# Performance work log

Hardware: AMD Instinct MI355X
Metric: run time of the kernel (lower is better)

The kernel has to match this reference:

```python
import jax, jax.numpy as jnp
import numpy as np

SEP_ID = 102  # bert-base [SEP]


def setup_inputs() -> dict:
    key = jax.random.key(0)
    B, S, H, M = 64, 512, 768, 21
    k1, k2, k3, k4 = jax.random.split(key, 4)
    hidden = jax.random.normal(k1, (B, S, H), dtype=jnp.float32)  # tf1 last_hidden_state
    ids = jax.random.randint(k2, (B, S), 1000, 30000)
    sep_pos = jnp.arange(24, 24 * (M + 1), 24)  # 21 sep positions < 512
    ids = ids.at[:, sep_pos].set(SEP_ID)
    W = jax.random.normal(k3, (H, H), dtype=jnp.float32) * 0.02  # nn.Linear weight [out,in]
    b = jnp.zeros((H,), dtype=jnp.float32)
    v = jax.random.normal(k4, (H,), dtype=jnp.float32) * 0.02    # linear_value [H,1] squeezed
    return {"hidden": hidden, "input_ids": ids, "W": W, "b": b, "v": v,
            "max_sent_count": M}


def _segment_attention_pool(hidden, input_ids, W, b, v, M):
    B, S, H = hidden.shape
    sep = input_ids == SEP_ID                                 # [B,S] bool
    csum = jnp.cumsum(sep.astype(jnp.int32), axis=1)
    seg = csum - sep.astype(jnp.int32)                        # seps strictly before t
    nsep = csum[:, -1]                                        # sentences per row
    pos = jnp.arange(S)
    # sentence k = tokens strictly between sep k-1 and sep k, excluding CLS (pos 0)
    valid = (~sep) & (pos[None, :] >= 1) & (seg < nsep[:, None]) & (seg < M)

    # attention scores: tanh(x @ W.T + b) @ v
    scores = jnp.einsum('bsh,h->bs', jnp.tanh(jnp.einsum('bsh,kh->bsk', hidden, W) + b), v)

    NS = B * M + 1                                            # +1 dummy segment for invalid tokens
    fid = jnp.where(valid, jnp.arange(B)[:, None] * M + seg, B * M).reshape(-1)
    sflat = jnp.where(valid, scores, -jnp.inf).reshape(-1)

    # per-segment stable softmax
    m = jax.ops.segment_max(sflat, fid, num_segments=NS)
    m = jnp.where(jnp.isfinite(m), m, 0.0)                    # empty segments
    e = jnp.where(valid.reshape(-1), jnp.exp(sflat - m[fid]), 0.0)
    denom = jax.ops.segment_sum(e, fid, num_segments=NS)
    w = e / jnp.where(denom[fid] > 0, denom[fid], 1.0)

    sent = jax.ops.segment_sum(w[:, None] * hidden.reshape(-1, H), fid,
                               num_segments=NS)[:B * M].reshape(B, M, H)
    # rows with zero sentences fall back to the CLS embedding (original behavior)
    sent = sent.at[:, 0, :].set(jnp.where((nsep == 0)[:, None], hidden[:, 0, :], sent[:, 0, :]))
    return sent


def reference(hidden, input_ids, W, b, v, max_sent_count):
    return _segment_attention_pool(hidden, input_ids, W, b, v, max_sent_count)
```

## Files before the change

### kernel.cpp

```cpp
#include <hip/hip_runtime.h>


#define SEP_ID 102
#define Bn 64
#define Sn 512
#define Hn 768
#define Mn 21
#define BS (Bn * Sn)

typedef __attribute__((ext_vector_type(8))) short bf16x8;
typedef __attribute__((ext_vector_type(8))) unsigned short u16x8;
typedef __attribute__((ext_vector_type(4))) float f32x4;

__device__ inline unsigned short f2bf(float x) {
  unsigned int u = __builtin_bit_cast(unsigned int, x);
  u += 0x7fffu + ((u >> 16) & 1u);
  return (unsigned short)(u >> 16);
}

__device__ inline u16x8 cvt8(float4 a, float4 b) {
  u16x8 r;
  r[0] = f2bf(a.x); r[1] = f2bf(a.y); r[2] = f2bf(a.z); r[3] = f2bf(a.w);
  r[4] = f2bf(b.x); r[5] = f2bf(b.y); r[6] = f2bf(b.z); r[7] = f2bf(b.w);
  return r;
}

__device__ inline float tanh_fast(float x) {
  float e = __builtin_amdgcn_exp2f(x * 2.885390081777927f);
  return 1.f - 2.f * __builtin_amdgcn_rcpf(e + 1.f);
}

__global__ void convw_kernel(const float* __restrict__ W, unsigned short* __restrict__ WBp) {
  int c = blockIdx.x * 256 + threadIdx.x;
  int nt = c / 1536;
  int r  = c % 1536;
  int ks = r >> 6;
  int ln = r & 63;
  int col = nt * 16 + (ln & 15);
  int k0  = ks * 32 + (ln >> 4) * 8;
  const float* src = &W[col * Hn + k0];
  float4 a = *reinterpret_cast<const float4*>(src);
  float4 b = *reinterpret_cast<const float4*>(src + 4);
  *reinterpret_cast<u16x8*>(&WBp[(size_t)c * 8]) = cvt8(a, b);
}

__global__ void segscan_kernel(const int* __restrict__ ids,
                               unsigned char* __restrict__ segv,
                               int* __restrict__ nsep) {
  int b = blockIdx.x;
  int s = threadIdx.x;
  __shared__ int cs[Sn];
  int sep = (ids[b * Sn + s] == SEP_ID) ? 1 : 0;
  cs[s] = sep;
  __syncthreads();
  for (int off = 1; off < Sn; off <<= 1) {
    int add = (s >= off) ? cs[s - off] : 0;
    __syncthreads();
    cs[s] += add;
    __syncthreads();
  }
  int csum = cs[s];
  int nb = cs[Sn - 1];
  int seg = csum - sep;
  bool valid = (!sep) && (s >= 1) && (seg < nb) && (seg < Mn);
  segv[b * Sn + s] = valid ? (unsigned char)seg : (unsigned char)0xFF;
  if (s == 0) nsep[b] = nb;
}

__global__ __launch_bounds__(1024, 4) void score_gemm_kernel(
    const float* __restrict__ hid, const unsigned short* __restrict__ WBp,
    const float* __restrict__ bbias, const float* __restrict__ vvec,
    float* __restrict__ scores) {
  __shared__ __align__(16) unsigned short As[64 * 768];
  __shared__ float scpart[16][64];

  const int t = threadIdx.x;
  const size_t rowBase = (size_t)blockIdx.x * 64;
  const int wid = t >> 6, lane = t & 63;
  const int l15 = lane & 15, l4 = lane >> 4;
  const int colBase = wid * 48;

  {
    const int srow = t >> 4;
    const int scloc = t & 15;
    const float* hsrc = &hid[(rowBase + srow) * Hn + scloc * 8];
    unsigned short* const arow = &As[srow * Hn];
    const int swz = srow & 7;
    float4 p[6][2];
#pragma unroll
    for (int cc = 0; cc < 6; ++cc) {
      p[cc][0] = *reinterpret_cast<const float4*>(hsrc + cc * 128);
      p[cc][1] = *reinterpret_cast<const float4*>(hsrc + cc * 128 + 4);
    }
#pragma unroll
    for (int cc = 0; cc < 6; ++cc)
      *reinterpret_cast<u16x8*>(arow + ((cc * 16 + scloc) ^ swz) * 8) =
          cvt8(p[cc][0], p[cc][1]);
  }
  __syncthreads();

  const unsigned short* const afrow = &As[l15 * Hn];
  const int aswz = l15 & 7;
  const unsigned short* bp0 = &WBp[((size_t)(wid * 3 + 0) * 24 * 64 + lane) * 8];
  const unsigned short* bp1 = &WBp[((size_t)(wid * 3 + 1) * 24 * 64 + lane) * 8];
  const unsigned short* bp2 = &WBp[((size_t)(wid * 3 + 2) * 24 * 64 + lane) * 8];

  f32x4 acc[4][3];
#pragma unroll
  for (int mi = 0; mi < 4; ++mi)
#pragma unroll
    for (int ni = 0; ni < 3; ++ni) acc[mi][ni] = (f32x4){0.f, 0.f, 0.f, 0.f};

  bf16x8 b0[3], b1[3], b2[3];
  b0[0] = *reinterpret_cast<const bf16x8*>(bp0);
  b0[1] = *reinterpret_cast<const bf16x8*>(bp1);
  b0[2] = *reinterpret_cast<const bf16x8*>(bp2);
  b1[0] = *reinterpret_cast<const bf16x8*>(bp0 + 512);
  b1[1] = *reinterpret_cast<const bf16x8*>(bp1 + 512);
  b1[2] = *reinterpret_cast<const bf16x8*>(bp2 + 512);

#pragma unroll
  for (int kk = 0; kk < 24; ++kk) {
    bf16x8 af[4];
#pragma unroll
    for (int mi = 0; mi < 4; ++mi)
      af[mi] = *reinterpret_cast<const bf16x8*>(
          &afrow[mi * 16 * Hn + (((kk * 4 + l4)) ^ aswz) * 8]);
    if (kk + 2 < 24) {
      b2[0] = *reinterpret_cast<const bf16x8*>(bp0 + (kk + 2) * 512);
      b2[1] = *reinterpret_cast<const bf16x8*>(bp1 + (kk + 2) * 512);
      b2[2] = *reinterpret_cast<const bf16x8*>(bp2 + (kk + 2) * 512);
    }
    __builtin_amdgcn_s_setprio(1);
#pragma unroll
    for (int mi = 0; mi < 4; ++mi)
#pragma unroll
      for (int ni = 0; ni < 3; ++ni)
        acc[mi][ni] = __builtin_amdgcn_mfma_f32_16x16x32_bf16(
            af[mi], b0[ni], acc[mi][ni], 0, 0, 0);
    __builtin_amdgcn_s_setprio(0);
#pragma unroll
    for (int ni = 0; ni < 3; ++ni) { b0[ni] = b1[ni]; b1[ni] = b2[ni]; }
  }

  float sc[4][4];
#pragma unroll
  for (int mi = 0; mi < 4; ++mi)
#pragma unroll
    for (int r = 0; r < 4; ++r) sc[mi][r] = 0.f;
#pragma unroll
  for (int ni = 0; ni < 3; ++ni) {
    int col = colBase + ni * 16 + l15;
    float vv = vvec[col];
    float bb = bbias[col];
#pragma unroll
    for (int mi = 0; mi < 4; ++mi)
#pragma unroll
      for (int r = 0; r < 4; ++r)
        sc[mi][r] += tanh_fast(acc[mi][ni][r] + bb) * vv;
  }
#pragma unroll
  for (int off = 1; off < 16; off <<= 1)
#pragma unroll
    for (int mi = 0; mi < 4; ++mi)
#pragma unroll
      for (int r = 0; r < 4; ++r)
        sc[mi][r] += __shfl_xor(sc[mi][r], off, 64);
  if (l15 == 0) {
#pragma unroll
    for (int mi = 0; mi < 4; ++mi)
#pragma unroll
      for (int r = 0; r < 4; ++r)
        scpart[wid][mi * 16 + l4 * 4 + r] = sc[mi][r];
  }
  __syncthreads();
  if (t < 64) {
    float s = 0.f;
#pragma unroll
    for (int w = 0; w < 16; ++w) s += scpart[w][t];
    scores[rowBase + t] = s;
  }
}

__global__ __launch_bounds__(256) void pool_kernel(
    const float* __restrict__ hid, const float* __restrict__ scores,
    const unsigned char* __restrict__ segv, const int* __restrict__ nsep,
    float* __restrict__ out) {
  int bm = blockIdx.x;
  int b = bm / Mn, m = bm % Mn;
  int t = threadIdx.x;
  __shared__ float wLds[Sn];
  __shared__ float red[256];
  __shared__ int ired[256];
  const float NEG = -1e30f;

  int base = b * Sn;
  unsigned char mg = (unsigned char)m;
  unsigned char g0 = segv[base + t], g1 = segv[base + 256 + t];
  bool v0 = (g0 == mg), v1 = (g1 == mg);
  float s0 = v0 ? scores[base + t] : NEG;
  float s1 = v1 ? scores[base + 256 + t] : NEG;

  red[t] = fmaxf(s0, s1);
  __syncthreads();
  for (int o = 128; o > 0; o >>= 1) {
    if (t < o) red[t] = fmaxf(red[t], red[t + o]);
    __syncthreads();
  }
  float gmax = red[0];
  __syncthreads();

  size_t obase = (size_t)bm * Hn;
  if (gmax <= -0.5e30f) {
    int nb = nsep[b];
    float a0 = 0.f, a1 = 0.f, a2 = 0.f;
    if (m == 0 && nb == 0) {
      const float* hp = hid + (size_t)base * Hn;
      a0 = hp[t]; a1 = hp[t + 256]; a2 = hp[t + 512];
    }
    out[obase + t] = a0; out[obase + 256 + t] = a1; out[obase + 512 + t] = a2;
    return;
  }

  float e0 = v0 ? expf(s0 - gmax) : 0.f;
  float e1 = v1 ? expf(s1 - gmax) : 0.f;
  red[t] = e0 + e1;
  __syncthreads();
  for (int o = 128; o > 0; o >>= 1) {
    if (t < o) red[t] += red[t + o];
    __syncthreads();
  }
  float inv = 1.f / red[0];
  __syncthreads();
  wLds[t] = e0 * inv;
  wLds[256 + t] = e1 * inv;

  ired[t] = min(v0 ? t : 0x7fffffff, v1 ? (256 + t) : 0x7fffffff);
  __syncthreads();
  for (int o = 128; o > 0; o >>= 1) {
    if (t < o) ired[t] = min(ired[t], ired[t + o]);
    __syncthreads();
  }
  int start = ired[0];
  __syncthreads();
  ired[t] = max(v0 ? t : -1, v1 ? (256 + t) : -1);
  __syncthreads();
  for (int o = 128; o > 0; o >>= 1) {
    if (t < o) ired[t] = max(ired[t], ired[t + o]);
    __syncthreads();
  }
  int end = ired[0];
  __syncthreads();

  float a0 = 0.f, a1 = 0.f, a2 = 0.f;
  for (int s = start; s <= end; ++s) {
    float w = wLds[s];
    if (w != 0.f) {
      const float* hp = hid + (size_t)(base + s) * Hn;
      a0 += w * hp[t];
      a1 += w * hp[t + 256];
      a2 += w * hp[t + 512];
    }
  }
  out[obase + t] = a0;
  out[obase + 256 + t] = a1;
  out[obase + 512 + t] = a2;
}

extern "C" void kernel_launch(void* const* d_in, const int* in_sizes, int n_in,
                              void* d_out, int out_size, void* d_ws, size_t ws_size,
                              hipStream_t stream) {
  const float* hidden = (const float*)d_in[0];
  const int* ids      = (const int*)d_in[1];
  const float* W      = (const float*)d_in[2];
  const float* bbias  = (const float*)d_in[3];
  const float* vvec   = (const float*)d_in[4];

  char* ws = (char*)d_ws;
  unsigned short* WBp  = (unsigned short*)(ws);
  float* scores        = (float*)(ws + 1179648);
  unsigned char* segv  = (unsigned char*)(ws + 1310720);
  int* nsep            = (int*)(ws + 1343488);

  convw_kernel<<<288, 256, 0, stream>>>(W, WBp);
  segscan_kernel<<<Bn, Sn, 0, stream>>>(ids, segv, nsep);
  score_gemm_kernel<<<BS / 64, 1024, 0, stream>>>(hidden, WBp, bbias, vvec, scores);
  pool_kernel<<<Bn * Mn, 256, 0, stream>>>(hidden, scores, segv, nsep, (float*)d_out);
}
```

Before: 78.03 us.

## Double-buffer A tiles in K chunks and process two row tiles per block

The score GEMM no longer stages the whole 64x768 A tile into LDS before computing. It now splits K into 256-wide chunks held in a double-buffered LDS array, prefetching the next chunk's fp32 hidden values into registers while MFMAs run on the current one. Each block also handles two 64-row tiles (grid shrinks from 512 to 256 blocks), so one block covers the whole 256 CUs and the pipeline continues across tiles. The goal is to hide global load latency and cut LDS use per block, at the cost of more barriers and a fixed grid tied to 256 CUs.

```diff
diff --git a/kernel.cpp b/kernel.cpp
--- a/kernel.cpp
+++ b/kernel.cpp
@@ -67,40 +67,77 @@
   if (s == 0) nsep[b] = nb;
 }
 
+__device__ inline void score_epilogue(f32x4 (&acc)[4][3],
+                                      const float* __restrict__ bbias,
+                                      const float* __restrict__ vvec,
+                                      float* __restrict__ scores,
+                                      float (*scpart)[64],
+                                      size_t rowBase, int wid, int l15, int l4,
+                                      int colBase, int t) {
+  float sc[4][4];
+#pragma unroll
+  for (int mi = 0; mi < 4; ++mi)
+#pragma unroll
+    for (int r = 0; r < 4; ++r) sc[mi][r] = 0.f;
+#pragma unroll
+  for (int ni = 0; ni < 3; ++ni) {
+    int col = colBase + ni * 16 + l15;
+    float vv = vvec[col];
+    float bb = bbias[col];
+#pragma unroll
+    for (int mi = 0; mi < 4; ++mi)
+#pragma unroll
+      for (int r = 0; r < 4; ++r)
+        sc[mi][r] += tanh_fast(acc[mi][ni][r] + bb) * vv;
+  }
+#pragma unroll
+  for (int off = 1; off < 16; off <<= 1)
+#pragma unroll
+    for (int mi = 0; mi < 4; ++mi)
+#pragma unroll
+      for (int r = 0; r < 4; ++r)
+        sc[mi][r] += __shfl_xor(sc[mi][r], off, 64);
+  if (l15 == 0) {
+#pragma unroll
+    for (int mi = 0; mi < 4; ++mi)
+#pragma unroll
+      for (int r = 0; r < 4; ++r)
+        scpart[wid][mi * 16 + l4 * 4 + r] = sc[mi][r];
+  }
+  __syncthreads();
+  if (t < 64) {
+    float s = 0.f;
+#pragma unroll
+    for (int w = 0; w < 16; ++w) s += scpart[w][t];
+    scores[rowBase + t] = s;
+  }
+}
+
 __global__ __launch_bounds__(1024, 4) void score_gemm_kernel(
     const float* __restrict__ hid, const unsigned short* __restrict__ WBp,
     const float* __restrict__ bbias, const float* __restrict__ vvec,
     float* __restrict__ scores) {
-  __shared__ __align__(16) unsigned short As[64 * 768];
+  __shared__ __align__(16) unsigned short As[2][64 * 256];
   __shared__ float scpart[16][64];
 
   const int t = threadIdx.x;
-  const size_t rowBase = (size_t)blockIdx.x * 64;
+  const size_t rb0 = (size_t)blockIdx.x * 64;
+  const size_t rb1 = (size_t)(blockIdx.x + 256) * 64;
+  const float* const h0 = hid + rb0 * Hn;
+  const float* const h1 = hid + rb1 * Hn;
   const int wid = t >> 6, lane = t & 63;
   const int l15 = lane & 15, l4 = lane >> 4;
   const int colBase = wid * 48;
 
-  {
-    const int srow = t >> 4;
-    const int scloc = t & 15;
-    const float* hsrc = &hid[(rowBase + srow) * Hn + scloc * 8];
-    unsigned short* const arow = &As[srow * Hn];
-    const int swz = srow & 7;
-    float4 p[6][2];
-#pragma unroll
-    for (int cc = 0; cc < 6; ++cc) {
-      p[cc][0] = *reinterpret_cast<const float4*>(hsrc + cc * 128);
-      p[cc][1] = *reinterpret_cast<const float4*>(hsrc + cc * 128 + 4);
-    }
-#pragma unroll
-    for (int cc = 0; cc < 6; ++cc)
-      *reinterpret_cast<u16x8*>(arow + ((cc * 16 + scloc) ^ swz) * 8) =
-          cvt8(p[cc][0], p[cc][1]);
-  }
-  __syncthreads();
-
-  const unsigned short* const afrow = &As[l15 * Hn];
+  const int srow = t >> 4;
+  const int ssl = t & 15;
+  const int sgoff = srow * Hn + ssl * 16;
+  const int wslot0 = (ssl * 2) ^ (srow & 7);
+  const int wslot1 = (ssl * 2 + 1) ^ (srow & 7);
+  unsigned short* const awr = &As[0][0] + srow * 256;
+
   const int aswz = l15 & 7;
+
   const unsigned short* bp0 = &WBp[((size_t)(wid * 3 + 0) * 24 * 64 + lane) * 8];
   const unsigned short* bp1 = &WBp[((size_t)(wid * 3 + 1) * 24 * 64 + lane) * 8];
   const unsigned short* bp2 = &WBp[((size_t)(wid * 3 + 2) * 24 * 64 + lane) * 8];
@@ -111,74 +148,79 @@
 #pragma unroll
     for (int ni = 0; ni < 3; ++ni) acc[mi][ni] = (f32x4){0.f, 0.f, 0.f, 0.f};
 
-  bf16x8 b0[3], b1[3], b2[3];
-  b0[0] = *reinterpret_cast<const bf16x8*>(bp0);
-  b0[1] = *reinterpret_cast<const bf16x8*>(bp1);
-  b0[2] = *reinterpret_cast<const bf16x8*>(bp2);
-  b1[0] = *reinterpret_cast<const bf16x8*>(bp0 + 512);
-  b1[1] = *reinterpret_cast<const bf16x8*>(bp1 + 512);
-  b1[2] = *reinterpret_cast<const bf16x8*>(bp2 + 512);
-
-#pragma unroll
-  for (int kk = 0; kk < 24; ++kk) {
-    bf16x8 af[4];
-#pragma unroll
-    for (int mi = 0; mi < 4; ++mi)
-      af[mi] = *reinterpret_cast<const bf16x8*>(
-          &afrow[mi * 16 * Hn + (((kk * 4 + l4)) ^ aswz) * 8]);
-    if (kk + 2 < 24) {
-      b2[0] = *reinterpret_cast<const bf16x8*>(bp0 + (kk + 2) * 512);
-      b2[1] = *reinterpret_cast<const bf16x8*>(bp1 + (kk + 2) * 512);
-      b2[2] = *reinterpret_cast<const bf16x8*>(bp2 + (kk + 2) * 512);
-    }
-    __builtin_amdgcn_s_setprio(1);
-#pragma unroll
-    for (int mi = 0; mi < 4; ++mi)
-#pragma unroll
-      for (int ni = 0; ni < 3; ++ni)
-        acc[mi][ni] = __builtin_amdgcn_mfma_f32_16x16x32_bf16(
-            af[mi], b0[ni], acc[mi][ni], 0, 0, 0);
-    __builtin_amdgcn_s_setprio(0);
-#pragma unroll
-    for (int ni = 0; ni < 3; ++ni) { b0[ni] = b1[ni]; b1[ni] = b2[ni]; }
-  }
-
-  float sc[4][4];
-#pragma unroll
-  for (int mi = 0; mi < 4; ++mi)
-#pragma unroll
-    for (int r = 0; r < 4; ++r) sc[mi][r] = 0.f;
-#pragma unroll
-  for (int ni = 0; ni < 3; ++ni) {
-    int col = colBase + ni * 16 + l15;
-    float vv = vvec[col];
-    float bb = bbias[col];
-#pragma unroll
-    for (int mi = 0; mi < 4; ++mi)
-#pragma unroll
-      for (int r = 0; r < 4; ++r)
-        sc[mi][r] += tanh_fast(acc[mi][ni][r] + bb) * vv;
-  }
-#pragma unroll
-  for (int off = 1; off < 16; off <<= 1)
-#pragma unroll
-    for (int mi = 0; mi < 4; ++mi)
-#pragma unroll
-      for (int r = 0; r < 4; ++r)
-        sc[mi][r] += __shfl_xor(sc[mi][r], off, 64);
-  if (l15 == 0) {
-#pragma unroll
-    for (int mi = 0; mi < 4; ++mi)
-#pragma unroll
-      for (int r = 0; r < 4; ++r)
-        scpart[wid][mi * 16 + l4 * 4 + r] = sc[mi][r];
-  }
-  __syncthreads();
-  if (t < 64) {
-    float s = 0.f;
-#pragma unroll
-    for (int w = 0; w < 16; ++w) s += scpart[w][t];
-    scores[rowBase + t] = s;
+  {
+    const float* hs = h0 + sgoff;
+    float4 a0 = *reinterpret_cast<const float4*>(hs);
+    float4 a1 = *reinterpret_cast<const float4*>(hs + 4);
+    float4 a2 = *reinterpret_cast<const float4*>(hs + 8);
+    float4 a3 = *reinterpret_cast<const float4*>(hs + 12);
+    *reinterpret_cast<u16x8*>(awr + wslot0 * 8) = cvt8(a0, a1);
+    *reinterpret_cast<u16x8*>(awr + wslot1 * 8) = cvt8(a2, a3);
+  }
+  bf16x8 bcur[3], bnxt[3];
+  bcur[0] = *reinterpret_cast<const bf16x8*>(bp0);
+  bcur[1] = *reinterpret_cast<const bf16x8*>(bp1);
+  bcur[2] = *reinterpret_cast<const bf16x8*>(bp2);
+  asm volatile("s_waitcnt lgkmcnt(0)" ::: "memory");
+  __builtin_amdgcn_s_barrier();
+  __builtin_amdgcn_sched_barrier(0);
+
+#pragma unroll
+  for (int c = 0; c < 6; ++c) {
+    float4 n0, n1, n2, n3;
+    if (c < 5) {
+      const float* hs = ((c + 1 < 3) ? h0 : h1) + sgoff + ((c + 1) % 3) * 256;
+      n0 = *reinterpret_cast<const float4*>(hs);
+      n1 = *reinterpret_cast<const float4*>(hs + 4);
+      n2 = *reinterpret_cast<const float4*>(hs + 8);
+      n3 = *reinterpret_cast<const float4*>(hs + 12);
+    }
+#pragma unroll
+    for (int ks = 0; ks < 8; ++ks) {
+      bf16x8 af[4];
+#pragma unroll
+      for (int mi = 0; mi < 4; ++mi)
+        af[mi] = *reinterpret_cast<const bf16x8*>(
+            &As[c & 1][mi * 4096 + l15 * 256 + (((ks * 4 + l4) ^ aswz)) * 8]);
+      const int cm = c % 3;
+      int kkn; bool have = true;
+      if (ks < 7) kkn = cm * 8 + ks + 1;
+      else if (cm < 2) kkn = cm * 8 + 8;
+      else { kkn = 0; have = (c != 5); }
+      if (have) {
+        bnxt[0] = *reinterpret_cast<const bf16x8*>(bp0 + kkn * 512);
+        bnxt[1] = *reinterpret_cast<const bf16x8*>(bp1 + kkn * 512);
+        bnxt[2] = *reinterpret_cast<const bf16x8*>(bp2 + kkn * 512);
+      }
+      __builtin_amdgcn_s_setprio(1);
+#pragma unroll
+      for (int mi = 0; mi < 4; ++mi)
+#pragma unroll
+        for (int ni = 0; ni < 3; ++ni)
+          acc[mi][ni] = __builtin_amdgcn_mfma_f32_16x16x32_bf16(
+              af[mi], bcur[ni], acc[mi][ni], 0, 0, 0);
+      __builtin_amdgcn_s_setprio(0);
+#pragma unroll
+      for (int ni = 0; ni < 3; ++ni) bcur[ni] = bnxt[ni];
+    }
+    if (c < 5) {
+      unsigned short* aw = &As[(c + 1) & 1][0] + srow * 256;
+      *reinterpret_cast<u16x8*>(aw + wslot0 * 8) = cvt8(n0, n1);
+      *reinterpret_cast<u16x8*>(aw + wslot1 * 8) = cvt8(n2, n3);
+    }
+    asm volatile("s_waitcnt lgkmcnt(0)" ::: "memory");
+    __builtin_amdgcn_s_barrier();
+    __builtin_amdgcn_sched_barrier(0);
+    if (c == 2 || c == 5) {
+      score_epilogue(acc, bbias, vvec, scores, scpart,
+                     (c == 2) ? rb0 : rb1, wid, l15, l4, colBase, t);
+      if (c == 2) {
+#pragma unroll
+        for (int mi = 0; mi < 4; ++mi)
+#pragma unroll
+          for (int ni = 0; ni < 3; ++ni) acc[mi][ni] = (f32x4){0.f, 0.f, 0.f, 0.f};
+      }
+    }
   }
 }
 
@@ -284,6 +326,6 @@
 
   convw_kernel<<<288, 256, 0, stream>>>(W, WBp);
   segscan_kernel<<<Bn, Sn, 0, stream>>>(ids, segv, nsep);
-  score_gemm_kernel<<<BS / 64, 1024, 0, stream>>>(hidden, WBp, bbias, vvec, scores);
+  score_gemm_kernel<<<256, 1024, 0, stream>>>(hidden, WBp, bbias, vvec, scores);
   pool_kernel<<<Bn * Mn, 256, 0, stream>>>(hidden, scores, segv, nsep, (float*)d_out);
 }
```

New measurement: 126.0 us. +61.5%, slower.
